# Kernel optimization log

Hardware: AMD Instinct MI355X
Metric: run time of the kernel (lower is better)

The kernel has to match this reference:

```python
import jax, jax.numpy as jnp
import numpy as np

KEEP_PROB = 0.3
KH, KW = 3, 3
STRIDE = (1, 1)
PADDING = ((1, 1), (1, 1))
DILATION = (1, 1)


def setup_inputs() -> dict:
    key = jax.random.key(0)
    k_x, k_w, k_m, k_b = jax.random.split(key, 4)
    B, C_in, H, W = 16, 64, 112, 112
    C_out = 128
    K = C_in * KH * KW  # 576
    x = jax.random.normal(k_x, (B, C_in, H, W), dtype=jnp.float32)
    weight = jax.random.normal(k_w, (C_out, K), dtype=jnp.float32)
    # binary sparsity pattern of the COO tensor, as a float mask
    mask = (jax.random.uniform(k_m, (C_out, K)) < KEEP_PROB).astype(jnp.float32)
    bias = jax.random.normal(k_b, (C_out,), dtype=jnp.float32)
    return {"x": x, "weight": weight, "mask": mask, "bias": bias}


def reference(x, weight, mask, bias):
    # Effective sparse weight matrix [C_out, C_in*kH*kW]
    spW = weight * mask
    # im2col (F.unfold): patches -> [B, C_in*kH*kW, H_out, W_out]
    # ordering of the K axis is (c, i, j) channel-major, matching torch unfold
    patches = jax.lax.conv_general_dilated_patches(
        x,
        filter_shape=(KH, KW),
        window_strides=STRIDE,
        padding=PADDING,
        rhs_dilation=DILATION,
    )  # [B, K, H_out, W_out]
    # sparse.mm(spW, X) + fold(1x1)  ==  GEMM over the K axis
    out = jnp.einsum('ok,bkhw->bohw', spW, patches)
    out = out + bias[None, :, None, None]
    return out
```

## Files before the change

### kernel.cpp

```cpp
#include <hip/hip_runtime.h>
#include <hip/hip_bf16.h>

#define C_IN    64
#define C_OUT   128
#define HH      112
#define WW      112
#define NB      16
#define KTOT    576
#define NSTEPS  36
#define NPIX    (HH*WW)
#define PH      114
#define PPIX    (PH*PH)
#define XT_OFF  147456
#define XT_BYTES ((size_t)NB * PPIX * C_IN * 2)
#define BAND_H  16
#define BH_X    18
#define B_RECS  324
#define A_BYTES 73728
#define B_BYTES 41472
#define TRB     51
#define TY      8
#define TX      16
#define HALO_X  18
#define HALO_P  180
#define TILES_X 7
#define NTILES  98

typedef __bf16 bf16x8 __attribute__((ext_vector_type(8)));
typedef float  f32x16 __attribute__((ext_vector_type(16)));

static __device__ __forceinline__ unsigned short f2bf(float v) {
    unsigned int u = __builtin_bit_cast(unsigned int, v);
    u = u + 0x7fffu + ((u >> 16) & 1u);
    return (unsigned short)(u >> 16);
}

#define GLOAD_LDS(gp, lp) __builtin_amdgcn_global_load_lds( \
    (const __attribute__((address_space(1))) void*)(gp),    \
    (__attribute__((address_space(3))) void*)(lp), 16, 0, 0)

__global__ __launch_bounds__(256) void prep_kernel(
        const float* __restrict__ weight, const float* __restrict__ mask,
        const float* __restrict__ x,
        unsigned short* __restrict__ pw, unsigned short* __restrict__ xT) {
    const int bx  = blockIdx.x;
    const int tid = threadIdx.x;
    if (bx < NSTEPS) {
        const int t  = bx;
        const int mt = tid >> 6;
        const int l  = tid & 63;
        const int g  = l >> 5;
        const int m  = mt * 32 + (l & 31);
        unsigned int words[4];
        #pragma unroll
        for (int ew = 0; ew < 4; ++ew) {
            unsigned int w2[2];
            #pragma unroll
            for (int h = 0; h < 2; ++h) {
                int e    = ew * 2 + h;
                int klog = t * 16 + g * 8 + e;
                int ij   = klog >> 6;
                int c    = klog & 63;
                int ko   = c * 9 + ij;
                w2[h] = f2bf(weight[m * KTOT + ko] * mask[m * KTOT + ko]);
            }
            words[ew] = w2[0] | (w2[1] << 16);
        }
        uint4 o4; o4.x = words[0]; o4.y = words[1]; o4.z = words[2]; o4.w = words[3];
        ((uint4*)pw)[(t * 4 + mt) * 64 + l] = o4;
    } else {
        const int idx = bx - NSTEPS;
        const int b   = idx / TRB;
        const int pp  = (idx % TRB) * 256 + tid;
        if (pp >= PPIX) return;
        const int hp = pp / PH, wp = pp - hp * PH;
        const int gh = hp - 1, gw = wp - 1;
        const bool valid = (unsigned)gh < (unsigned)HH && (unsigned)gw < (unsigned)WW;
        const float* src = x + (size_t)b * C_IN * (HH * WW) + (gh * WW + gw);
        uint4* dst = (uint4*)(xT + ((size_t)b * PPIX + pp) * C_IN);
        #pragma unroll
        for (int cb = 0; cb < 8; ++cb) {
            unsigned int w4[4];
            #pragma unroll
            for (int h = 0; h < 4; ++h) {
                float v0 = valid ? src[(size_t)(cb * 8 + h * 2    ) * (HH * WW)] : 0.0f;
                float v1 = valid ? src[(size_t)(cb * 8 + h * 2 + 1) * (HH * WW)] : 0.0f;
                w4[h] = (unsigned)f2bf(v0) | ((unsigned)f2bf(v1) << 16);
            }
            uint4 o; o.x = w4[0]; o.y = w4[1]; o.z = w4[2]; o.w = w4[3];
            dst[cb] = o;
        }
    }
}

__global__ __launch_bounds__(256, 1) void sparse_conv_band_kernel(
        const unsigned short* __restrict__ xT, const unsigned short* __restrict__ pw,
        const float* __restrict__ bias, float* __restrict__ out) {
    __shared__ __align__(16) unsigned char smem[A_BYTES + 2 * B_BYTES];
    unsigned char* As  = smem;
    unsigned char* Bs0 = smem + A_BYTES;
    unsigned char* Bs1 = smem + A_BYTES + B_BYTES;

    const int bid  = (blockIdx.x & 7) * 28 + (blockIdx.x >> 3);
    const int b    = bid / 14;
    const int rem  = bid % 14;
    const int mh   = rem & 1;
    const int band = rem >> 1;
    const int h0   = band * BAND_H;
    const int tid  = threadIdx.x;
    const int wave = tid >> 6, l = tid & 63;
    const int g = l >> 5, ln = l & 31;

    const char* xTb = (const char*)xT + (size_t)b * PPIX * (C_IN * 2);
    const char* pwb = (const char*)pw;

    {
        #pragma unroll
        for (int r = 0; r < 18; ++r) {
            int c  = r * 256 + tid;
            int t  = c >> 7;
            int mt = (c >> 6) & 1;
            int ll = c & 63;
            const char* gp = pwb + (size_t)((t * 4 + mh * 2 + mt) * 64 + ll) * 16;
            GLOAD_LDS(gp, (char*)As + r * 4096 + wave * 1024);
        }
    }

    auto STAGE = [&](int it, unsigned char* dst) {
        const int w0 = it * 16;
        #pragma unroll
        for (int r = 0; r < 10; ++r) {
            int chunk = r * 256 + tid;
            int p = chunk >> 3, s = chunk & 7;
            int yy = p / BH_X, xx = p - yy * BH_X;
            const char* gp = xTb + (size_t)((h0 + yy) * PH + (w0 + xx)) * (C_IN * 2)
                                 + (((s ^ p) & 7) << 4);
            GLOAD_LDS(gp, (char*)dst + r * 4096 + wave * 1024);
        }
        if (tid < 32) {
            int chunk = 10 * 256 + tid;
            int p = chunk >> 3, s = chunk & 7;
            int yy = p / BH_X, xx = p - yy * BH_X;
            const char* gp = xTb + (size_t)((h0 + yy) * PH + (w0 + xx)) * (C_IN * 2)
                                 + (((s ^ p) & 7) << 4);
            GLOAD_LDS(gp, (char*)dst + 10 * 4096);
        }
    };

    const int px = ln & 15;
    const int pyb = 4 * wave + (ln >> 4);

    float bv[2][16];
    #pragma unroll
    for (int mt = 0; mt < 2; ++mt)
        #pragma unroll
        for (int r = 0; r < 16; ++r) {
            int mloc = (r & 3) + 8 * (r >> 2) + 4 * g;
            bv[mt][r] = bias[mh * 64 + mt * 32 + mloc];
        }

    STAGE(0, Bs0);
    __syncthreads();

    const size_t outb = (size_t)b * C_OUT * NPIX;

    #pragma unroll 1
    for (int it = 0; it < 7; ++it) {
        unsigned char* curB = (it & 1) ? Bs1 : Bs0;
        unsigned char* nxtB = (it & 1) ? Bs0 : Bs1;
        if (it < 6) STAGE(it + 1, nxtB);

        f32x16 acc[2][2];
        #pragma unroll
        for (int mt = 0; mt < 2; ++mt)
            #pragma unroll
            for (int ntp = 0; ntp < 2; ++ntp)
                #pragma unroll
                for (int r = 0; r < 16; ++r) acc[mt][ntp][r] = bv[mt][r];

        #pragma unroll
        for (int t = 0; t < NSTEPS; ++t) {
            const int ij = t >> 2, cs = t & 3;
            const int di = ij / 3, dj = ij - di * 3;
            const int jb = cs * 2 + g;
            bf16x8 a0 = __builtin_bit_cast(bf16x8,
                *(const uint4*)(As + ((t * 2 + 0) * 64 + l) * 16));
            bf16x8 a1 = __builtin_bit_cast(bf16x8,
                *(const uint4*)(As + ((t * 2 + 1) * 64 + l) * 16));
            #pragma unroll
            for (int ntp = 0; ntp < 2; ++ntp) {
                const int Pa = (pyb + 2 * ntp + di) * BH_X + (px + dj);
                bf16x8 bb = __builtin_bit_cast(bf16x8,
                    *(const uint4*)(curB + Pa * 128 + (((jb ^ Pa) & 7) << 4)));
                acc[0][ntp] = __builtin_amdgcn_mfma_f32_32x32x16_bf16(a0, bb, acc[0][ntp], 0, 0, 0);
                acc[1][ntp] = __builtin_amdgcn_mfma_f32_32x32x16_bf16(a1, bb, acc[1][ntp], 0, 0, 0);
            }
        }

        #pragma unroll
        for (int mt = 0; mt < 2; ++mt)
            #pragma unroll
            for (int r = 0; r < 16; ++r) {
                int mloc = (r & 3) + 8 * (r >> 2) + 4 * g;
                int o = mh * 64 + mt * 32 + mloc;
                #pragma unroll
                for (int ntp = 0; ntp < 2; ++ntp) {
                    int row = h0 + pyb + 2 * ntp;
                    out[outb + (size_t)o * NPIX + row * WW + it * 16 + px] = acc[mt][ntp][r];
                }
            }

        if (it < 6) {
            asm volatile("s_waitcnt vmcnt(56)" ::: "memory");
            __builtin_amdgcn_sched_barrier(0);
            __builtin_amdgcn_s_barrier();
        }
    }
}

__global__ __launch_bounds__(256, 4) void sparse_conv_fb_kernel(
        const float* __restrict__ x, const unsigned short* __restrict__ pw,
        const float* __restrict__ bias, float* __restrict__ out) {
    __shared__ __align__(16) unsigned short xs[HALO_P * C_IN];

    const int bid = blockIdx.x;
    const int b   = bid / NTILES;
    const int t98 = bid % NTILES;
    const int tyi = t98 / TILES_X;
    const int txi = t98 % TILES_X;
    const int h0  = tyi * TY, w0 = txi * TX;
    const int tid = threadIdx.x;

    const float* xb = x + (size_t)b * C_IN * HH * WW;
    {
        const int p  = tid;
        const bool act = p < HALO_P;
        int yy = p / HALO_X;
        int xx = p - yy * HALO_X;
        int gh = h0 + yy - 1, gw = w0 + xx - 1;
        const bool valid = act && (unsigned)gh < (unsigned)HH && (unsigned)gw < (unsigned)WW;
        const float* bp = xb + (gh * WW + gw);
        float v[C_IN];
        #pragma unroll
        for (int c = 0; c < C_IN; ++c)
            v[c] = valid ? bp[c * (HH * WW)] : 0.0f;
        if (act) {
            char* xc = (char*)xs + p * (C_IN * 2);
            #pragma unroll
            for (int j = 0; j < 8; ++j) {
                bf16x8 bvv;
                #pragma unroll
                for (int e = 0; e < 8; ++e) bvv[e] = (__bf16)v[j * 8 + e];
                *(uint4*)(xc + (((j ^ p) & 7) << 4)) = __builtin_bit_cast(uint4, bvv);
            }
        }
    }
    __syncthreads();

    const int wave = tid >> 6, l = tid & 63;
    const int wm = wave >> 1, wn = wave & 1;
    const int g  = l >> 5,  ln = l & 31;

    int P0[2];
    #pragma unroll
    for (int ntp = 0; ntp < 2; ++ntp) {
        int pt = wn * 64 + ntp * 32 + ln;
        P0[ntp] = (pt >> 4) * HALO_X + (pt & 15);
    }

    f32x16 acc[2][2];
    #pragma unroll
    for (int i = 0; i < 2; ++i)
        #pragma unroll
        for (int jq = 0; jq < 2; ++jq)
            #pragma unroll
            for (int q = 0; q < 16; ++q) acc[i][jq][q] = 0.0f;

    const uint4* __restrict__ pwv = (const uint4*)pw;

    #pragma unroll 1
    for (int ij = 0; ij < 9; ++ij) {
        const int di = ij / 3;
        const int dj = ij - di * 3;
        const int P0a = P0[0] + di * HALO_X + dj;
        const int P1a = P0[1] + di * HALO_X + dj;
        #pragma unroll
        for (int cs = 0; cs < 4; ++cs) {
            const int t = ij * 4 + cs;
            bf16x8 a0 = __builtin_bit_cast(bf16x8, pwv[(t * 4 + wm * 2 + 0) * 64 + l]);
            bf16x8 a1 = __builtin_bit_cast(bf16x8, pwv[(t * 4 + wm * 2 + 1) * 64 + l]);
            const int jb = cs * 2 + g;
            bf16x8 b0 = __builtin_bit_cast(bf16x8,
                *(const uint4*)((const char*)xs + P0a * (C_IN * 2) + (((jb ^ P0a) & 7) << 4)));
            bf16x8 b1 = __builtin_bit_cast(bf16x8,
                *(const uint4*)((const char*)xs + P1a * (C_IN * 2) + (((jb ^ P1a) & 7) << 4)));
            acc[0][0] = __builtin_amdgcn_mfma_f32_32x32x16_bf16(a0, b0, acc[0][0], 0, 0, 0);
            acc[0][1] = __builtin_amdgcn_mfma_f32_32x32x16_bf16(a0, b1, acc[0][1], 0, 0, 0);
            acc[1][0] = __builtin_amdgcn_mfma_f32_32x32x16_bf16(a1, b0, acc[1][0], 0, 0, 0);
            acc[1][1] = __builtin_amdgcn_mfma_f32_32x32x16_bf16(a1, b1, acc[1][1], 0, 0, 0);
        }
    }

    const size_t outb = (size_t)b * C_OUT * HH * WW;
    #pragma unroll
    for (int mtp = 0; mtp < 2; ++mtp) {
        #pragma unroll
        for (int r = 0; r < 16; ++r) {
            int mloc = (r & 3) + 8 * (r >> 2) + 4 * g;
            int o = (wm * 2 + mtp) * 32 + mloc;
            float bvv = bias[o];
            #pragma unroll
            for (int ntp = 0; ntp < 2; ++ntp) {
                int p  = wn * 64 + ntp * 32 + ln;
                int gh = h0 + (p >> 4), gw = w0 + (p & 15);
                out[outb + ((size_t)o * HH + gh) * WW + gw] = acc[mtp][ntp][r] + bvv;
            }
        }
    }
}

extern "C" void kernel_launch(void* const* d_in, const int* in_sizes, int n_in,
                              void* d_out, int out_size, void* d_ws, size_t ws_size,
                              hipStream_t stream) {
    const float* x    = (const float*)d_in[0];
    const float* w    = (const float*)d_in[1];
    const float* mk   = (const float*)d_in[2];
    const float* bs   = (const float*)d_in[3];
    float* out        = (float*)d_out;
    unsigned short* pw = (unsigned short*)d_ws;

    if (ws_size >= (size_t)XT_OFF + XT_BYTES) {
        unsigned short* xT = (unsigned short*)((char*)d_ws + XT_OFF);
        prep_kernel<<<dim3(NSTEPS + NB * TRB), dim3(256), 0, stream>>>(w, mk, x, pw, xT);
        sparse_conv_band_kernel<<<dim3(224), dim3(256), 0, stream>>>(xT, pw, bs, out);
    } else {
        prep_kernel<<<dim3(NSTEPS), dim3(256), 0, stream>>>(w, mk, x, pw, (unsigned short*)pw);
        sparse_conv_fb_kernel<<<dim3(NB * NTILES), dim3(256), 0, stream>>>(x, pw, bs, out);
    }
}
```

Before: 74.30 us.

## Split output channels into quarters per block and single-buffer the input band

Each block now computes 32 output channels instead of 64, which doubles the grid to 448 blocks and halves the weight tile held in LDS. The B input tile drops from double to single buffering: the next stage is issued after a barrier that follows compute, and its loads overlap with the output stores. LDS use per block falls enough that two blocks fit per CU, aiming for better occupancy and latency hiding. The cost is that every input band is loaded twice as often, and less of the global-load latency overlaps with MFMA work.

Result: faster. 67.98 us (-8.5%).

```diff
diff --git a/kernel.cpp b/kernel.cpp
--- a/kernel.cpp
+++ b/kernel.cpp
@@ -16,7 +16,7 @@
 #define BAND_H  16
 #define BH_X    18
 #define B_RECS  324
-#define A_BYTES 73728
+#define A_BYTES 36864
 #define B_BYTES 41472
 #define TRB     51
 #define TY      8
@@ -93,19 +93,18 @@
     }
 }
 
-__global__ __launch_bounds__(256, 1) void sparse_conv_band_kernel(
+__global__ __launch_bounds__(256, 2) void sparse_conv_mq_kernel(
         const unsigned short* __restrict__ xT, const unsigned short* __restrict__ pw,
         const float* __restrict__ bias, float* __restrict__ out) {
-    __shared__ __align__(16) unsigned char smem[A_BYTES + 2 * B_BYTES];
-    unsigned char* As  = smem;
-    unsigned char* Bs0 = smem + A_BYTES;
-    unsigned char* Bs1 = smem + A_BYTES + B_BYTES;
-
-    const int bid  = (blockIdx.x & 7) * 28 + (blockIdx.x >> 3);
-    const int b    = bid / 14;
-    const int rem  = bid % 14;
-    const int mh   = rem & 1;
-    const int band = rem >> 1;
+    __shared__ __align__(16) unsigned char smem[A_BYTES + B_BYTES];
+    unsigned char* As = smem;
+    unsigned char* Bs = smem + A_BYTES;
+
+    const int bid  = (blockIdx.x & 7) * 56 + (blockIdx.x >> 3);
+    const int b    = bid / 28;
+    const int rem  = bid % 28;
+    const int mq   = rem & 3;
+    const int band = rem >> 2;
     const int h0   = band * BAND_H;
     const int tid  = threadIdx.x;
     const int wave = tid >> 6, l = tid & 63;
@@ -116,17 +115,16 @@
 
     {
         #pragma unroll
-        for (int r = 0; r < 18; ++r) {
+        for (int r = 0; r < 9; ++r) {
             int c  = r * 256 + tid;
-            int t  = c >> 7;
-            int mt = (c >> 6) & 1;
+            int t  = c >> 6;
             int ll = c & 63;
-            const char* gp = pwb + (size_t)((t * 4 + mh * 2 + mt) * 64 + ll) * 16;
+            const char* gp = pwb + (size_t)((t * 4 + mq) * 64 + ll) * 16;
             GLOAD_LDS(gp, (char*)As + r * 4096 + wave * 1024);
         }
     }
 
-    auto STAGE = [&](int it, unsigned char* dst) {
+    auto STAGE = [&](int it) {
         const int w0 = it * 16;
         #pragma unroll
         for (int r = 0; r < 10; ++r) {
@@ -135,7 +133,7 @@
             int yy = p / BH_X, xx = p - yy * BH_X;
             const char* gp = xTb + (size_t)((h0 + yy) * PH + (w0 + xx)) * (C_IN * 2)
                                  + (((s ^ p) & 7) << 4);
-            GLOAD_LDS(gp, (char*)dst + r * 4096 + wave * 1024);
+            GLOAD_LDS(gp, (char*)Bs + r * 4096 + wave * 1024);
         }
         if (tid < 32) {
             int chunk = 10 * 256 + tid;
@@ -143,75 +141,65 @@
             int yy = p / BH_X, xx = p - yy * BH_X;
             const char* gp = xTb + (size_t)((h0 + yy) * PH + (w0 + xx)) * (C_IN * 2)
                                  + (((s ^ p) & 7) << 4);
-            GLOAD_LDS(gp, (char*)dst + 10 * 4096);
+            GLOAD_LDS(gp, (char*)Bs + 10 * 4096);
         }
     };
 
     const int px = ln & 15;
     const int pyb = 4 * wave + (ln >> 4);
 
-    float bv[2][16];
+    float bv[16];
     #pragma unroll
-    for (int mt = 0; mt < 2; ++mt)
-        #pragma unroll
-        for (int r = 0; r < 16; ++r) {
-            int mloc = (r & 3) + 8 * (r >> 2) + 4 * g;
-            bv[mt][r] = bias[mh * 64 + mt * 32 + mloc];
-        }
-
-    STAGE(0, Bs0);
+    for (int r = 0; r < 16; ++r) {
+        int mloc = (r & 3) + 8 * (r >> 2) + 4 * g;
+        bv[r] = bias[mq * 32 + mloc];
+    }
+
+    STAGE(0);
     __syncthreads();
 
     const size_t outb = (size_t)b * C_OUT * NPIX;
 
     #pragma unroll 1
     for (int it = 0; it < 7; ++it) {
-        unsigned char* curB = (it & 1) ? Bs1 : Bs0;
-        unsigned char* nxtB = (it & 1) ? Bs0 : Bs1;
-        if (it < 6) STAGE(it + 1, nxtB);
-
-        f32x16 acc[2][2];
-        #pragma unroll
-        for (int mt = 0; mt < 2; ++mt)
-            #pragma unroll
-            for (int ntp = 0; ntp < 2; ++ntp)
-                #pragma unroll
-                for (int r = 0; r < 16; ++r) acc[mt][ntp][r] = bv[mt][r];
+        f32x16 acc[2];
+        #pragma unroll
+        for (int ntp = 0; ntp < 2; ++ntp)
+            #pragma unroll
+            for (int r = 0; r < 16; ++r) acc[ntp][r] = bv[r];
 
         #pragma unroll
         for (int t = 0; t < NSTEPS; ++t) {
             const int ij = t >> 2, cs = t & 3;
             const int di = ij / 3, dj = ij - di * 3;
             const int jb = cs * 2 + g;
-            bf16x8 a0 = __builtin_bit_cast(bf16x8,
-                *(const uint4*)(As + ((t * 2 + 0) * 64 + l) * 16));
-            bf16x8 a1 = __builtin_bit_cast(bf16x8,
-                *(const uint4*)(As + ((t * 2 + 1) * 64 + l) * 16));
+            bf16x8 a = __builtin_bit_cast(bf16x8,
+                *(const uint4*)(As + ((size_t)(t * 64 + l)) * 16));
             #pragma unroll
             for (int ntp = 0; ntp < 2; ++ntp) {
                 const int Pa = (pyb + 2 * ntp + di) * BH_X + (px + dj);
                 bf16x8 bb = __builtin_bit_cast(bf16x8,
-                    *(const uint4*)(curB + Pa * 128 + (((jb ^ Pa) & 7) << 4)));
-                acc[0][ntp] = __builtin_amdgcn_mfma_f32_32x32x16_bf16(a0, bb, acc[0][ntp], 0, 0, 0);
-                acc[1][ntp] = __builtin_amdgcn_mfma_f32_32x32x16_bf16(a1, bb, acc[1][ntp], 0, 0, 0);
-            }
-        }
-
-        #pragma unroll
-        for (int mt = 0; mt < 2; ++mt)
-            #pragma unroll
-            for (int r = 0; r < 16; ++r) {
-                int mloc = (r & 3) + 8 * (r >> 2) + 4 * g;
-                int o = mh * 64 + mt * 32 + mloc;
-                #pragma unroll
-                for (int ntp = 0; ntp < 2; ++ntp) {
-                    int row = h0 + pyb + 2 * ntp;
-                    out[outb + (size_t)o * NPIX + row * WW + it * 16 + px] = acc[mt][ntp][r];
-                }
-            }
+                    *(const uint4*)(Bs + Pa * 128 + (((jb ^ Pa) & 7) << 4)));
+                acc[ntp] = __builtin_amdgcn_mfma_f32_32x32x16_bf16(a, bb, acc[ntp], 0, 0, 0);
+            }
+        }
+
+        __builtin_amdgcn_s_barrier();
+        if (it < 6) STAGE(it + 1);
+
+        #pragma unroll
+        for (int r = 0; r < 16; ++r) {
+            int mloc = (r & 3) + 8 * (r >> 2) + 4 * g;
+            int o = mq * 32 + mloc;
+            #pragma unroll
+            for (int ntp = 0; ntp < 2; ++ntp) {
+                int row = h0 + pyb + 2 * ntp;
+                out[outb + (size_t)o * NPIX + row * WW + it * 16 + px] = acc[ntp][r];
+            }
+        }
 
         if (it < 6) {
-            asm volatile("s_waitcnt vmcnt(56)" ::: "memory");
+            asm volatile("s_waitcnt vmcnt(32)" ::: "memory");
             __builtin_amdgcn_sched_barrier(0);
             __builtin_amdgcn_s_barrier();
         }
@@ -332,7 +320,7 @@
     if (ws_size >= (size_t)XT_OFF + XT_BYTES) {
         unsigned short* xT = (unsigned short*)((char*)d_ws + XT_OFF);
         prep_kernel<<<dim3(NSTEPS + NB * TRB), dim3(256), 0, stream>>>(w, mk, x, pw, xT);
-        sparse_conv_band_kernel<<<dim3(224), dim3(256), 0, stream>>>(xT, pw, bs, out);
+        sparse_conv_mq_kernel<<<dim3(448), dim3(256), 0, stream>>>(xT, pw, bs, out);
     } else {
         prep_kernel<<<dim3(NSTEPS), dim3(256), 0, stream>>>(w, mk, x, pw, (unsigned short*)pw);
         sparse_conv_fb_kernel<<<dim3(NB * NTILES), dim3(256), 0, stream>>>(x, pw, bs, out);
```

## Read im2col B operands directly from global in channel-block-major layout

Applied to the files above, without the earlier changes.

Changes the padded bf16 activation layout to channel-block-major (8 blocks of 8 channels per pixel plane) and drops LDS staging of activation bands. The main kernel now loads B fragments straight from global/L2 into registers with a two-step software prefetch, and iterates over contiguous linear pixel chunks instead of 16x16 spatial bands. LDS use falls to the weight tile only, and launch bounds allow two blocks per CU. The cost is that the 9x overlapping halo reads now go through the cache hierarchy instead of LDS reuse, and the prefetch distance may not hide global latency.

Result: slower. 185.2 us (+149.3%).

```diff
diff --git a/kernel.cpp b/kernel.cpp
--- a/kernel.cpp
+++ b/kernel.cpp
@@ -12,12 +12,8 @@
 #define PH      114
 #define PPIX    (PH*PH)
 #define XT_OFF  147456
-#define XT_BYTES ((size_t)NB * PPIX * C_IN * 2)
-#define BAND_H  16
-#define BH_X    18
-#define B_RECS  324
+#define XT_BYTES ((size_t)NB * 8 * PPIX * 16)
 #define A_BYTES 73728
-#define B_BYTES 41472
 #define TRB     51
 #define TY      8
 #define TX      16
@@ -77,7 +73,7 @@
         const int gh = hp - 1, gw = wp - 1;
         const bool valid = (unsigned)gh < (unsigned)HH && (unsigned)gw < (unsigned)WW;
         const float* src = x + (size_t)b * C_IN * (HH * WW) + (gh * WW + gw);
-        uint4* dst = (uint4*)(xT + ((size_t)b * PPIX + pp) * C_IN);
+        uint4* dst = (uint4*)xT;
         #pragma unroll
         for (int cb = 0; cb < 8; ++cb) {
             unsigned int w4[4];
@@ -88,30 +84,26 @@
                 w4[h] = (unsigned)f2bf(v0) | ((unsigned)f2bf(v1) << 16);
             }
             uint4 o; o.x = w4[0]; o.y = w4[1]; o.z = w4[2]; o.w = w4[3];
-            dst[cb] = o;
-        }
-    }
-}
-
-__global__ __launch_bounds__(256, 1) void sparse_conv_band_kernel(
+            dst[((size_t)b * 8 + cb) * PPIX + pp] = o;
+        }
+    }
+}
+
+__global__ __launch_bounds__(256, 2) void sparse_conv_bl2_kernel(
         const unsigned short* __restrict__ xT, const unsigned short* __restrict__ pw,
         const float* __restrict__ bias, float* __restrict__ out) {
-    __shared__ __align__(16) unsigned char smem[A_BYTES + 2 * B_BYTES];
-    unsigned char* As  = smem;
-    unsigned char* Bs0 = smem + A_BYTES;
-    unsigned char* Bs1 = smem + A_BYTES + B_BYTES;
+    __shared__ __align__(16) unsigned char As[A_BYTES];
 
     const int bid  = (blockIdx.x & 7) * 28 + (blockIdx.x >> 3);
     const int b    = bid / 14;
     const int rem  = bid % 14;
-    const int mh   = rem & 1;
-    const int band = rem >> 1;
-    const int h0   = band * BAND_H;
+    const int mh   = rem / 7;
+    const int blk  = rem % 7;
     const int tid  = threadIdx.x;
     const int wave = tid >> 6, l = tid & 63;
     const int g = l >> 5, ln = l & 31;
 
-    const char* xTb = (const char*)xT + (size_t)b * PPIX * (C_IN * 2);
+    const char* xTb = (const char*)xT + (size_t)b * 8 * PPIX * 16;
     const char* pwb = (const char*)pw;
 
     {
@@ -126,30 +118,6 @@
         }
     }
 
-    auto STAGE = [&](int it, unsigned char* dst) {
-        const int w0 = it * 16;
-        #pragma unroll
-        for (int r = 0; r < 10; ++r) {
-            int chunk = r * 256 + tid;
-            int p = chunk >> 3, s = chunk & 7;
-            int yy = p / BH_X, xx = p - yy * BH_X;
-            const char* gp = xTb + (size_t)((h0 + yy) * PH + (w0 + xx)) * (C_IN * 2)
-                                 + (((s ^ p) & 7) << 4);
-            GLOAD_LDS(gp, (char*)dst + r * 4096 + wave * 1024);
-        }
-        if (tid < 32) {
-            int chunk = 10 * 256 + tid;
-            int p = chunk >> 3, s = chunk & 7;
-            int yy = p / BH_X, xx = p - yy * BH_X;
-            const char* gp = xTb + (size_t)((h0 + yy) * PH + (w0 + xx)) * (C_IN * 2)
-                                 + (((s ^ p) & 7) << 4);
-            GLOAD_LDS(gp, (char*)dst + 10 * 4096);
-        }
-    };
-
-    const int px = ln & 15;
-    const int pyb = 4 * wave + (ln >> 4);
-
     float bv[2][16];
     #pragma unroll
     for (int mt = 0; mt < 2; ++mt)
@@ -159,16 +127,20 @@
             bv[mt][r] = bias[mh * 64 + mt * 32 + mloc];
         }
 
-    STAGE(0, Bs0);
     __syncthreads();
 
     const size_t outb = (size_t)b * C_OUT * NPIX;
 
     #pragma unroll 1
-    for (int it = 0; it < 7; ++it) {
-        unsigned char* curB = (it & 1) ? Bs1 : Bs0;
-        unsigned char* nxtB = (it & 1) ? Bs0 : Bs1;
-        if (it < 6) STAGE(it + 1, nxtB);
+    for (int gi = 0; gi < 7; ++gi) {
+        const int p0 = ((blk * 7 + gi) * 4 + wave) * 64;
+        int rec0[2];
+        #pragma unroll
+        for (int ntp = 0; ntp < 2; ++ntp) {
+            int p = p0 + ntp * 32 + ln;
+            int h = p / WW;
+            rec0[ntp] = h * PH + (p - h * WW);
+        }
 
         f32x16 acc[2][2];
         #pragma unroll
@@ -178,23 +150,38 @@
                 #pragma unroll
                 for (int r = 0; r < 16; ++r) acc[mt][ntp][r] = bv[mt][r];
 
+        uint4 Bb[2][2];
+        #pragma unroll
+        for (int t = 0; t < 2; ++t) {
+            const int ij = t >> 2, cs = t & 3;
+            const int off = (ij / 3) * PH + (ij % 3);
+            #pragma unroll
+            for (int ntp = 0; ntp < 2; ++ntp)
+                Bb[t][ntp] = *(const uint4*)(xTb
+                    + ((size_t)(cs * 2 + g) * PPIX + rec0[ntp] + off) * 16);
+        }
+
         #pragma unroll
         for (int t = 0; t < NSTEPS; ++t) {
-            const int ij = t >> 2, cs = t & 3;
-            const int di = ij / 3, dj = ij - di * 3;
-            const int jb = cs * 2 + g;
+            bf16x8 b0 = __builtin_bit_cast(bf16x8, Bb[t & 1][0]);
+            bf16x8 b1 = __builtin_bit_cast(bf16x8, Bb[t & 1][1]);
+            if (t + 2 < NSTEPS) {
+                const int t2 = t + 2;
+                const int ij2 = t2 >> 2, cs2 = t2 & 3;
+                const int off2 = (ij2 / 3) * PH + (ij2 % 3);
+                #pragma unroll
+                for (int ntp = 0; ntp < 2; ++ntp)
+                    Bb[t & 1][ntp] = *(const uint4*)(xTb
+                        + ((size_t)(cs2 * 2 + g) * PPIX + rec0[ntp] + off2) * 16);
+            }
             bf16x8 a0 = __builtin_bit_cast(bf16x8,
                 *(const uint4*)(As + ((t * 2 + 0) * 64 + l) * 16));
             bf16x8 a1 = __builtin_bit_cast(bf16x8,
                 *(const uint4*)(As + ((t * 2 + 1) * 64 + l) * 16));
-            #pragma unroll
-            for (int ntp = 0; ntp < 2; ++ntp) {
-                const int Pa = (pyb + 2 * ntp + di) * BH_X + (px + dj);
-                bf16x8 bb = __builtin_bit_cast(bf16x8,
-                    *(const uint4*)(curB + Pa * 128 + (((jb ^ Pa) & 7) << 4)));
-                acc[0][ntp] = __builtin_amdgcn_mfma_f32_32x32x16_bf16(a0, bb, acc[0][ntp], 0, 0, 0);
-                acc[1][ntp] = __builtin_amdgcn_mfma_f32_32x32x16_bf16(a1, bb, acc[1][ntp], 0, 0, 0);
-            }
+            acc[0][0] = __builtin_amdgcn_mfma_f32_32x32x16_bf16(a0, b0, acc[0][0], 0, 0, 0);
+            acc[0][1] = __builtin_amdgcn_mfma_f32_32x32x16_bf16(a0, b1, acc[0][1], 0, 0, 0);
+            acc[1][0] = __builtin_amdgcn_mfma_f32_32x32x16_bf16(a1, b0, acc[1][0], 0, 0, 0);
+            acc[1][1] = __builtin_amdgcn_mfma_f32_32x32x16_bf16(a1, b1, acc[1][1], 0, 0, 0);
         }
 
         #pragma unroll
@@ -204,17 +191,9 @@
                 int mloc = (r & 3) + 8 * (r >> 2) + 4 * g;
                 int o = mh * 64 + mt * 32 + mloc;
                 #pragma unroll
-                for (int ntp = 0; ntp < 2; ++ntp) {
-                    int row = h0 + pyb + 2 * ntp;
-                    out[outb + (size_t)o * NPIX + row * WW + it * 16 + px] = acc[mt][ntp][r];
-                }
-            }
-
-        if (it < 6) {
-            asm volatile("s_waitcnt vmcnt(56)" ::: "memory");
-            __builtin_amdgcn_sched_barrier(0);
-            __builtin_amdgcn_s_barrier();
-        }
+                for (int ntp = 0; ntp < 2; ++ntp)
+                    out[outb + (size_t)o * NPIX + p0 + ntp * 32 + ln] = acc[mt][ntp][r];
+            }
     }
 }
 
@@ -332,7 +311,7 @@
     if (ws_size >= (size_t)XT_OFF + XT_BYTES) {
         unsigned short* xT = (unsigned short*)((char*)d_ws + XT_OFF);
         prep_kernel<<<dim3(NSTEPS + NB * TRB), dim3(256), 0, stream>>>(w, mk, x, pw, xT);
-        sparse_conv_band_kernel<<<dim3(224), dim3(256), 0, stream>>>(xT, pw, bs, out);
+        sparse_conv_bl2_kernel<<<dim3(224), dim3(256), 0, stream>>>(xT, pw, bs, out);
     } else {
         prep_kernel<<<dim3(NSTEPS), dim3(256), 0, stream>>>(w, mk, x, pw, (unsigned short*)pw);
         sparse_conv_fb_kernel<<<dim3(NB * NTILES), dim3(256), 0, stream>>>(x, pw, bs, out);
```
